# Optimization experiments

Measured on AMD Instinct MI355X. Metric: run time of the kernel, lower is better.

Reference implementation:

```python
import jax, jax.numpy as jnp
import numpy as np

# dims (see shape_source): seq S = d_t+1 must equal d_k for the unary quantum loader
B, T, D_IN = 128, 127, 48
DK = 128
S = T + 1            # tokens incl. class token; S == DK
H, L = 8, 6
P = (S * S - S) // 2  # RBS angles per head (pyramid circuit over S wires)


def _pyramid_pairs(n):
    # deterministic pyramid ordering of n(n-1)/2 adjacent-pair Givens rotations
    a, b = [], []
    for k in range(n - 1):
        for i in range(k, -1, -1):
            a.append(i)
            b.append(i + 1)
    return np.asarray(a, np.int32), np.asarray(b, np.int32)


def _build_W(phi, pa, pb, n):
    # classical simulation of the RBS pyramid circuit restricted to the unary
    # subspace: product of Givens rotations -> orthogonal n x n matrix
    def step(W, inp):
        ia, ib, th = inp
        c, s = jnp.cos(th), jnp.sin(th)
        ra, rb = W[ia], W[ib]
        W = W.at[ia].set(c * ra - s * rb)
        W = W.at[ib].set(s * ra + c * rb)
        return W, None
    W0 = jnp.eye(n, dtype=phi.dtype)
    W, _ = jax.lax.scan(step, W0, (pa, pb, phi))
    return W


def _layer_norm(x, g, b, eps=1e-5):
    m = jnp.mean(x, axis=-1, keepdims=True)
    v = jnp.mean((x - m) ** 2, axis=-1, keepdims=True)
    return (x - m) * jax.lax.rsqrt(v + eps) * g + b


def setup_inputs() -> dict:
    key = jax.random.key(0)
    ks = jax.random.split(key, 8)
    f32 = jnp.float32
    return {
        "x": jax.random.normal(ks[0], (B, T, D_IN), f32),
        "embed_w": jax.random.normal(ks[1], (DK, D_IN), f32) / np.sqrt(D_IN),
        "embed_b": jnp.zeros((DK,), f32),
        "class_token": jax.random.normal(ks[2], (DK,), f32) / DK,
        "norm0_g": jnp.ones((DK,), f32),
        "norm0_b": jnp.zeros((DK,), f32),
        "Vw": jax.random.normal(ks[3], (L, H, DK, DK), f32) / np.sqrt(DK),
        "Vb": jnp.zeros((L, H, DK), f32),
        "ln_g": jnp.ones((L, H, DK), f32),
        "ln_b": jnp.zeros((L, H, DK), f32),
        "phi": jax.random.normal(ks[4], (L, H, P), f32) / np.sqrt(S),
        "merger_w": jax.random.normal(ks[5], (L, H), f32) / np.sqrt(H),
        "merger_b": jnp.zeros((L,), f32),
    }


def reference(x, embed_w, embed_b, class_token, norm0_g, norm0_b,
              Vw, Vb, ln_g, ln_b, phi, merger_w, merger_b):
    Bsz = x.shape[0]
    pa, pb = _pyramid_pairs(S)
    # orthogonal score matrices for every (layer, head)
    Ws = jax.vmap(lambda p: _build_W(p, pa, pb, S))(phi.reshape(L * H, P))
    Ws = Ws.reshape(L, H, S, S)

    # embed patches, prepend class token (pos_embedding add is a no-op in the
    # original source: bare `+self.pos_embedding` statement, so it is omitted)
    tok = jnp.einsum('btf,df->btd', x, embed_w) + embed_b
    h = jnp.concatenate([jnp.broadcast_to(class_token, (Bsz, 1, DK)), tok], axis=1)
    h = _layer_norm(h, norm0_g, norm0_b)

    scale = 1.0 / np.sqrt(DK)
    for l in range(L):
        nrm = jnp.sqrt(jnp.sum(h * h, axis=-1))      # input3: token norms [B,S]
        u = h / nrm[..., None]                        # unit tokens (convert_array)
        hh, nn, uu = h, nrm, u

        def head(W, vw, vb, g, be):
            V = jnp.einsum('bsd,ed->bse', hh, vw) + vb
            M = jnp.einsum('bsd,de,bte->bst', uu, W, uu)
            A = (M * M) * (nn[:, :, None] * nn[:, None, :])
            Pm = jax.nn.softmax(A * scale, axis=-1)
            return _layer_norm(jnp.einsum('bst,btd->bsd', Pm, V) + hh, g, be)

        hs = jax.vmap(head)(Ws[l], Vw[l], Vb[l], ln_g[l], ln_b[l])  # [H,B,S,D]
        h = jnp.einsum('hbsd,h->bsd', hs, merger_w[l]) + merger_b[l]
    return h[:, -1, :]
```

## Files before the change

### kernel.cpp

```cpp
#include <hip/hip_runtime.h>
#include <hip/hip_bf16.h>


typedef __bf16 bf16x8 __attribute__((ext_vector_type(8)));
typedef float  f32x4  __attribute__((ext_vector_type(4)));
typedef unsigned int u32;

#define LDH 136

__global__ void __launch_bounds__(256)
vw_bf16_kernel(const float* __restrict__ vw, __bf16* __restrict__ cvw)
{
    int i = (blockIdx.x * 256 + threadIdx.x) * 4;
#pragma unroll
    for (int j = 0; j < 4; j++) cvw[i + j] = (__bf16)vw[i + j];
}

__global__ void __launch_bounds__(64)
sincos_kernel(const float* __restrict__ phi, float2* __restrict__ csn)
{
    const int mat = blockIdx.x / 254;
    const int t   = blockIdx.x % 254;
    const int j   = threadIdx.x;

    float th = 0.f;
    if (t < 253) {
        const int p = t & 1, i = 2 * j + p;
        const int lim = min(t, 252 - t);
        if (i <= lim) {
            const int k = (t + i) >> 1;
            th = phi[mat * 8128 + ((k * (k + 1)) >> 1) + (k - i)];
        }
    }
    float sn, cs;
    __sincosf(th, &sn, &cs);
    csn[(mat * 254 + t) * 64 + j] = make_float2(cs, sn);
}

__global__ void __launch_bounds__(64)
build_w_kernel(const float2* __restrict__ csn, __bf16* __restrict__ wt)
{
    const int mat = blockIdx.x >> 4;
    const int grp = blockIdx.x & 15;
    const int c0  = grp * 8;
    const int lam = threadIdx.x;

    const float2* base = csn + (mat * 254) * 64 + lam;

    float vlo[8], vhi[8];
#pragma unroll
    for (int j = 0; j < 8; j++) {
        vlo[j] = (2 * lam     == c0 + j) ? 1.f : 0.f;
        vhi[j] = (2 * lam + 1 == c0 + j) ? 1.f : 0.f;
    }

    float2 a  = base[0];
    float2 bq = base[64];

    for (int t = 0; t < 252; t += 2) {
        float2 c2 = base[(t + 2) * 64];
        float2 d2 = base[(t + 3) * 64];

        {
            const float cs = a.x, sn = a.y;
#pragma unroll
            for (int j = 0; j < 8; j++) {
                float lo = vlo[j], hi = vhi[j];
                vlo[j] = cs * lo - sn * hi;
                vhi[j] = sn * lo + cs * hi;
            }
        }
        {
            const float cs = bq.x, sn = bq.y;
#pragma unroll
            for (int j = 0; j < 8; j++) {
                float y  = __shfl_down(vlo[j], 1);
                float x  = vhi[j];
                float xn = cs * x - sn * y;
                float yn = sn * x + cs * y;
                vhi[j] = xn;
                float z = __shfl_up(yn, 1);
                if (lam > 0) vlo[j] = z;
            }
        }
        a = c2; bq = d2;
    }
    {
        const float cs = a.x, sn = a.y;
#pragma unroll
        for (int j = 0; j < 8; j++) {
            float lo = vlo[j], hi = vhi[j];
            vlo[j] = cs * lo - sn * hi;
            vhi[j] = sn * lo + cs * hi;
        }
    }

    u32* wtu = (u32*)wt;
#pragma unroll
    for (int j = 0; j < 8; j++) {
        __bf16 va = (__bf16)vlo[j];
        __bf16 vb = (__bf16)vhi[j];
        u32 pk = (u32)__builtin_bit_cast(unsigned short, va)
               | ((u32)__builtin_bit_cast(unsigned short, vb) << 16);
        wtu[mat * 8192 + (c0 + j) * 64 + lam] = pk;
    }
}

static __device__ __forceinline__ float block_sum_128(float v, float* sred)
{
#pragma unroll
    for (int m = 32; m; m >>= 1) v += __shfl_xor(v, m);
    __syncthreads();
    if ((threadIdx.x & 63) == 0) sred[threadIdx.x >> 6] = v;
    __syncthreads();
    return sred[0] + sred[1];
}

__global__ void __launch_bounds__(128)
embed_kernel(const float* __restrict__ x,  const float* __restrict__ ew,
             const float* __restrict__ eb, const float* __restrict__ ct,
             const float* __restrict__ g0, const float* __restrict__ b0,
             float* __restrict__ hf, __bf16* __restrict__ hb, float* __restrict__ invn)
{
    __shared__ float sx[48];
    __shared__ float sred[2];
    const int b = blockIdx.x & 127, s = blockIdx.x >> 7, d = threadIdx.x;

    float val;
    if (s == 0) {
        val = ct[d];
    } else {
        if (d < 48) sx[d] = x[(b * 127 + (s - 1)) * 48 + d];
        __syncthreads();
        float aa = 0.f;
#pragma unroll
        for (int f = 0; f < 48; f++) aa = fmaf(sx[f], ew[d * 48 + f], aa);
        val = aa + eb[d];
    }
    float mean = block_sum_128(val, sred) * (1.f / 128.f);
    float xc   = val - mean;
    float var  = block_sum_128(xc * xc, sred) * (1.f / 128.f);
    float y    = xc * rsqrtf(var + 1e-5f) * g0[d] + b0[d];
    float ss   = block_sum_128(y * y, sred);

    const int o = (b * 128 + s) * 128 + d;
    hf[o] = y;
    hb[o] = (__bf16)y;
    if (d == 0) invn[b * 128 + s] = rsqrtf(ss);
}

__global__ void __launch_bounds__(512, 2)
attn_kernel(int l,
            const float*  __restrict__ hf,  const __bf16* __restrict__ hb,
            const float*  __restrict__ invn, const __bf16* __restrict__ wt,
            const __bf16* __restrict__ vw,  const float* __restrict__ vb,
            const float* __restrict__ lng,  const float* __restrict__ lnb,
            const float* __restrict__ mwp,  __bf16* __restrict__ hs)
{
    __shared__ __align__(16) __bf16 sH[128 * LDH];
    __shared__ __align__(16) __bf16 sB[128 * LDH];
    __shared__ __align__(16) __bf16 sT[128 * LDH];
    __shared__ float sInv[128];
    __shared__ float sVb[128];
    __shared__ float sLg[128];
    __shared__ float sLb[128];

    const int tid  = threadIdx.x;
    const int lane = tid & 63, wave = tid >> 6;
    const int l15  = lane & 15, quad = lane >> 4;
    const int b    = blockIdx.x & 127;
    const int hh   = blockIdx.x >> 7;
    const int lh   = l * 8 + hh;

    const __bf16* hbp = hb + b * 16384;
    const __bf16* wtp = wt + lh * 16384;
    const __bf16* vwp = vw + lh * 16384;

    bf16x8 vwr[4];
#pragma unroll
    for (int c = 0; c < 4; c++) {
        int ch  = tid + c * 512;
        int row = ch >> 4, cc = ch & 15;
        bf16x8 hv = *(const bf16x8*)(hbp + ch * 8);
        bf16x8 wv = *(const bf16x8*)(wtp + ch * 8);
        vwr[c]    = *(const bf16x8*)(vwp + ch * 8);
        *(bf16x8*)(&sH[row * LDH + cc * 8]) = hv;
        *(bf16x8*)(&sB[row * LDH + cc * 8]) = wv;
    }
    if (tid < 128) {
        sInv[tid] = invn[b * 128 + tid];
        sVb[tid]  = vb[lh * 128 + tid];
        sLg[tid]  = lng[lh * 128 + tid];
        sLb[tid]  = lnb[lh * 128 + tid];
    }
    __syncthreads();

    const int rowA = wave * 16 + l15;
    const int kq   = quad * 8;
    const int srow = wave * 16 + quad * 4;
    const f32x4 vzero = {0.f, 0.f, 0.f, 0.f};

    f32x4 acc[8];

#pragma unroll
    for (int t = 0; t < 8; t++) acc[t] = vzero;
#pragma unroll
    for (int k0 = 0; k0 < 128; k0 += 32) {
        bf16x8 af = *(const bf16x8*)(&sH[rowA * LDH + k0 + kq]);
#pragma unroll
        for (int t = 0; t < 8; t++) {
            bf16x8 bfr = *(const bf16x8*)(&sB[(t * 16 + l15) * LDH + k0 + kq]);
            acc[t] = __builtin_amdgcn_mfma_f32_16x16x32_bf16(af, bfr, acc[t], 0, 0, 0);
        }
    }
#pragma unroll
    for (int t = 0; t < 8; t++)
#pragma unroll
        for (int r = 0; r < 4; r++)
            sT[(srow + r) * LDH + t * 16 + l15] = (__bf16)acc[t][r];

    __syncthreads();

#pragma unroll
    for (int c = 0; c < 4; c++) {
        int ch = tid + c * 512; int row = ch >> 4, cc = ch & 15;
        *(bf16x8*)(&sB[row * LDH + cc * 8]) = vwr[c];
    }

#pragma unroll
    for (int t = 0; t < 8; t++) acc[t] = vzero;
#pragma unroll
    for (int k0 = 0; k0 < 128; k0 += 32) {
        bf16x8 af = *(const bf16x8*)(&sT[rowA * LDH + k0 + kq]);
#pragma unroll
        for (int t = 0; t < 8; t++) {
            bf16x8 bfr = *(const bf16x8*)(&sH[(t * 16 + l15) * LDH + k0 + kq]);
            acc[t] = __builtin_amdgcn_mfma_f32_16x16x32_bf16(af, bfr, acc[t], 0, 0, 0);
        }
    }

    {
        const float scale = 0.08838834764831843f;
        float invs[4], invt[8];
#pragma unroll
        for (int r = 0; r < 4; r++) invs[r] = sInv[srow + r];
#pragma unroll
        for (int t = 0; t < 8; t++) invt[t] = sInv[t * 16 + l15];

        float mx[4] = {-3e38f, -3e38f, -3e38f, -3e38f};
#pragma unroll
        for (int t = 0; t < 8; t++)
#pragma unroll
            for (int r = 0; r < 4; r++) {
                float g = acc[t][r];
                float v = g * g * invs[r] * invt[t] * scale;
                acc[t][r] = v;
                mx[r] = fmaxf(mx[r], v);
            }
#pragma unroll
        for (int m = 1; m < 16; m <<= 1)
#pragma unroll
            for (int r = 0; r < 4; r++) mx[r] = fmaxf(mx[r], __shfl_xor(mx[r], m));

        float sm[4] = {0.f, 0.f, 0.f, 0.f};
#pragma unroll
        for (int t = 0; t < 8; t++)
#pragma unroll
            for (int r = 0; r < 4; r++) {
                float e = __expf(acc[t][r] - mx[r]);
                acc[t][r] = e;
                sm[r] += e;
            }
#pragma unroll
        for (int m = 1; m < 16; m <<= 1)
#pragma unroll
            for (int r = 0; r < 4; r++) sm[r] += __shfl_xor(sm[r], m);
#pragma unroll
        for (int r = 0; r < 4; r++) sm[r] = 1.0f / sm[r];
#pragma unroll
        for (int t = 0; t < 8; t++)
#pragma unroll
            for (int r = 0; r < 4; r++)
                sT[(srow + r) * LDH + t * 16 + l15] = (__bf16)(acc[t][r] * sm[r]);
    }

    float hres[8][4];
    {
        const float* hfp = hf + (b * 128 + srow) * 128;
#pragma unroll
        for (int t = 0; t < 8; t++)
#pragma unroll
            for (int r = 0; r < 4; r++)
                hres[t][r] = hfp[r * 128 + t * 16 + l15];
    }

    __syncthreads();

#pragma unroll
    for (int t = 0; t < 8; t++) acc[t] = vzero;
#pragma unroll
    for (int k0 = 0; k0 < 128; k0 += 32) {
        bf16x8 af = *(const bf16x8*)(&sH[rowA * LDH + k0 + kq]);
#pragma unroll
        for (int t = 0; t < 8; t++) {
            bf16x8 bfr = *(const bf16x8*)(&sB[(t * 16 + l15) * LDH + k0 + kq]);
            acc[t] = __builtin_amdgcn_mfma_f32_16x16x32_bf16(af, bfr, acc[t], 0, 0, 0);
        }
    }
    __syncthreads();

    {
        float vbv[8];
#pragma unroll
        for (int t = 0; t < 8; t++) vbv[t] = sVb[t * 16 + l15];
#pragma unroll
        for (int t = 0; t < 8; t++)
#pragma unroll
            for (int r = 0; r < 4; r++)
                sH[(t * 16 + l15) * LDH + srow + r] = (__bf16)(acc[t][r] + vbv[t]);
    }
    __syncthreads();

#pragma unroll
    for (int t = 0; t < 8; t++) acc[t] = vzero;
#pragma unroll
    for (int k0 = 0; k0 < 128; k0 += 32) {
        bf16x8 af = *(const bf16x8*)(&sT[rowA * LDH + k0 + kq]);
#pragma unroll
        for (int t = 0; t < 8; t++) {
            bf16x8 bfr = *(const bf16x8*)(&sH[(t * 16 + l15) * LDH + k0 + kq]);
            acc[t] = __builtin_amdgcn_mfma_f32_16x16x32_bf16(af, bfr, acc[t], 0, 0, 0);
        }
    }

    {
        const float mw = mwp[lh];
        float sum_[4] = {0.f, 0.f, 0.f, 0.f};
        float sq_[4]  = {0.f, 0.f, 0.f, 0.f};
#pragma unroll
        for (int t = 0; t < 8; t++)
#pragma unroll
            for (int r = 0; r < 4; r++) {
                float x = acc[t][r] + hres[t][r];
                acc[t][r] = x;
                sum_[r] += x;
                sq_[r]  += x * x;
            }
#pragma unroll
        for (int m = 1; m < 16; m <<= 1)
#pragma unroll
            for (int r = 0; r < 4; r++) {
                sum_[r] += __shfl_xor(sum_[r], m);
                sq_[r]  += __shfl_xor(sq_[r], m);
            }
        float mean[4], rstd[4];
#pragma unroll
        for (int r = 0; r < 4; r++) {
            mean[r] = sum_[r] * (1.f / 128.f);
            float var = sq_[r] * (1.f / 128.f) - mean[r] * mean[r];
            rstd[r] = rsqrtf(fmaxf(var, 0.f) + 1e-5f);
        }
        float lgv[8], lbv[8];
#pragma unroll
        for (int t = 0; t < 8; t++) {
            lgv[t] = sLg[t * 16 + l15];
            lbv[t] = sLb[t * 16 + l15];
        }
        __bf16* hsp = hs + ((hh * 128 + b) * 128 + srow) * 128;
#pragma unroll
        for (int t = 0; t < 8; t++)
#pragma unroll
            for (int r = 0; r < 4; r++) {
                float y = (acc[t][r] - mean[r]) * rstd[r] * lgv[t] + lbv[t];
                hsp[r * 128 + t * 16 + l15] = (__bf16)(y * mw);
            }
    }
}

__global__ void __launch_bounds__(128)
merge_kernel(const __bf16* __restrict__ hs, const float* __restrict__ mbp, int l,
             float* __restrict__ hf, __bf16* __restrict__ hb, float* __restrict__ invn,
             float* __restrict__ out, int last)
{
    __shared__ float sred[2];
    const int b = blockIdx.x & 127, s = blockIdx.x >> 7, d = threadIdx.x;

    float acc = mbp[l];
#pragma unroll
    for (int h = 0; h < 8; h++)
        acc += (float)hs[((h * 128 + b) * 128 + s) * 128 + d];

    float ss = block_sum_128(acc * acc, sred);

    const int o = (b * 128 + s) * 128 + d;
    hf[o] = acc;
    hb[o] = (__bf16)acc;
    if (d == 0) invn[b * 128 + s] = rsqrtf(ss);
    if (last && s == 127) out[b * 128 + d] = acc;
}

extern "C" void kernel_launch(void* const* d_in, const int* in_sizes, int n_in,
                              void* d_out, int out_size, void* d_ws, size_t ws_size,
                              hipStream_t stream)
{
    (void)in_sizes; (void)n_in; (void)out_size; (void)ws_size;

    const float* x   = (const float*)d_in[0];
    const float* ew  = (const float*)d_in[1];
    const float* eb  = (const float*)d_in[2];
    const float* ct  = (const float*)d_in[3];
    const float* g0  = (const float*)d_in[4];
    const float* b0  = (const float*)d_in[5];
    const float* vw  = (const float*)d_in[6];
    const float* vb  = (const float*)d_in[7];
    const float* lng = (const float*)d_in[8];
    const float* lnb = (const float*)d_in[9];
    const float* phi = (const float*)d_in[10];
    const float* mw  = (const float*)d_in[11];
    const float* mb  = (const float*)d_in[12];
    float* out = (float*)d_out;

    char* ws = (char*)d_ws;
    __bf16* wt   = (__bf16*)(ws);
    float*  hf   = (float*)(ws + 1572864);
    __bf16* hb   = (__bf16*)(ws + 9961472);
    float*  invn = (float*)(ws + 14155776);
    __bf16* hs   = (__bf16*)(ws + 14221312);
    __bf16* cvw  = (__bf16*)(ws + 47775744);
    float2* csn  = (float2*)(ws + 49348608);

    vw_bf16_kernel<<<768, 256, 0, stream>>>(vw, cvw);
    sincos_kernel<<<48 * 254, 64, 0, stream>>>(phi, csn);
    build_w_kernel<<<768, 64, 0, stream>>>(csn, wt);
    embed_kernel<<<16384, 128, 0, stream>>>(x, ew, eb, ct, g0, b0, hf, hb, invn);
    for (int l = 0; l < 6; l++) {
        attn_kernel<<<1024, 512, 0, stream>>>(l, hf, hb, invn, wt, cvw, vb,
                                              lng, lnb, mw, hs);
        merge_kernel<<<16384, 128, 0, stream>>>(hs, mb, l, hf, hb, invn, out,
                                                (l == 5) ? 1 : 0);
    }
}
```

Baseline: 470.5 us.

## Use 4-wave blocks with 32-row tiles, XOR-swizzled LDS, and head-major block order

The attention kernel now runs with 256 threads, and each wave computes two 16-row MFMA tiles that share every B-fragment load, halving B reads from LDS per MFMA. The padded LDS layout is replaced by an XOR swizzle to avoid bank conflicts without padding. Block indexing is changed so the 8 heads of one batch run in adjacent blocks, which should improve L2 reuse of hb/hf. In exchange there are fewer waves per block and more accumulator registers per thread (hres and acc both double), which may reduce occupancy.

After: 533.4 us. 13.4% more time.

```diff
diff --git a/kernel.cpp b/kernel.cpp
--- a/kernel.cpp
+++ b/kernel.cpp
@@ -6,7 +6,10 @@
 typedef float  f32x4  __attribute__((ext_vector_type(4)));
 typedef unsigned int u32;
 
-#define LDH 136
+__device__ __forceinline__ int sidx(int row, int col)
+{
+    return row * 128 + ((((col >> 3) ^ (row & 15)) << 3) | (col & 7));
+}
 
 __global__ void __launch_bounds__(256)
 vw_bf16_kernel(const float* __restrict__ vw, __bf16* __restrict__ cvw)
@@ -60,7 +63,6 @@
     for (int t = 0; t < 252; t += 2) {
         float2 c2 = base[(t + 2) * 64];
         float2 d2 = base[(t + 3) * 64];
-
         {
             const float cs = a.x, sn = a.y;
 #pragma unroll
@@ -149,7 +151,7 @@
     if (d == 0) invn[b * 128 + s] = rsqrtf(ss);
 }
 
-__global__ void __launch_bounds__(512, 2)
+__global__ void __launch_bounds__(256, 1)
 attn_kernel(int l,
             const float*  __restrict__ hf,  const __bf16* __restrict__ hb,
             const float*  __restrict__ invn, const __bf16* __restrict__ wt,
@@ -157,35 +159,35 @@
             const float* __restrict__ lng,  const float* __restrict__ lnb,
             const float* __restrict__ mwp,  __bf16* __restrict__ hs)
 {
-    __shared__ __align__(16) __bf16 sH[128 * LDH];
-    __shared__ __align__(16) __bf16 sB[128 * LDH];
-    __shared__ __align__(16) __bf16 sT[128 * LDH];
+    __shared__ __align__(16) __bf16 sH[128 * 128];
+    __shared__ __align__(16) __bf16 sB[128 * 128];
+    __shared__ __align__(16) __bf16 sT[128 * 128];
     __shared__ float sInv[128];
     __shared__ float sVb[128];
     __shared__ float sLg[128];
     __shared__ float sLb[128];
 
     const int tid  = threadIdx.x;
-    const int lane = tid & 63, wave = tid >> 6;
+    const int lane = tid & 63, w = tid >> 6;
     const int l15  = lane & 15, quad = lane >> 4;
-    const int b    = blockIdx.x & 127;
-    const int hh   = blockIdx.x >> 7;
+    const int hh   = blockIdx.x & 7;
+    const int b    = blockIdx.x >> 3;
     const int lh   = l * 8 + hh;
 
     const __bf16* hbp = hb + b * 16384;
     const __bf16* wtp = wt + lh * 16384;
     const __bf16* vwp = vw + lh * 16384;
 
-    bf16x8 vwr[4];
-#pragma unroll
-    for (int c = 0; c < 4; c++) {
-        int ch  = tid + c * 512;
+    bf16x8 vwr[8];
+#pragma unroll
+    for (int c = 0; c < 8; c++) {
+        int ch  = tid + c * 256;
         int row = ch >> 4, cc = ch & 15;
         bf16x8 hv = *(const bf16x8*)(hbp + ch * 8);
         bf16x8 wv = *(const bf16x8*)(wtp + ch * 8);
         vwr[c]    = *(const bf16x8*)(vwp + ch * 8);
-        *(bf16x8*)(&sH[row * LDH + cc * 8]) = hv;
-        *(bf16x8*)(&sB[row * LDH + cc * 8]) = wv;
+        *(bf16x8*)(&sH[sidx(row, cc * 8)]) = hv;
+        *(bf16x8*)(&sB[sidx(row, cc * 8)]) = wv;
     }
     if (tid < 128) {
         sInv[tid] = invn[b * 128 + tid];
@@ -195,118 +197,116 @@
     }
     __syncthreads();
 
-    const int rowA = wave * 16 + l15;
+    const int r0   = w * 32;
     const int kq   = quad * 8;
-    const int srow = wave * 16 + quad * 4;
+    const int q4   = quad * 4;
     const f32x4 vzero = {0.f, 0.f, 0.f, 0.f};
 
-    f32x4 acc[8];
-
-#pragma unroll
-    for (int t = 0; t < 8; t++) acc[t] = vzero;
-#pragma unroll
-    for (int k0 = 0; k0 < 128; k0 += 32) {
-        bf16x8 af = *(const bf16x8*)(&sH[rowA * LDH + k0 + kq]);
-#pragma unroll
-        for (int t = 0; t < 8; t++) {
-            bf16x8 bfr = *(const bf16x8*)(&sB[(t * 16 + l15) * LDH + k0 + kq]);
-            acc[t] = __builtin_amdgcn_mfma_f32_16x16x32_bf16(af, bfr, acc[t], 0, 0, 0);
-        }
-    }
-#pragma unroll
-    for (int t = 0; t < 8; t++)
-#pragma unroll
-        for (int r = 0; r < 4; r++)
-            sT[(srow + r) * LDH + t * 16 + l15] = (__bf16)acc[t][r];
-
-    __syncthreads();
-
-#pragma unroll
-    for (int c = 0; c < 4; c++) {
-        int ch = tid + c * 512; int row = ch >> 4, cc = ch & 15;
-        *(bf16x8*)(&sB[row * LDH + cc * 8]) = vwr[c];
-    }
-
-#pragma unroll
-    for (int t = 0; t < 8; t++) acc[t] = vzero;
-#pragma unroll
-    for (int k0 = 0; k0 < 128; k0 += 32) {
-        bf16x8 af = *(const bf16x8*)(&sT[rowA * LDH + k0 + kq]);
-#pragma unroll
-        for (int t = 0; t < 8; t++) {
-            bf16x8 bfr = *(const bf16x8*)(&sH[(t * 16 + l15) * LDH + k0 + kq]);
-            acc[t] = __builtin_amdgcn_mfma_f32_16x16x32_bf16(af, bfr, acc[t], 0, 0, 0);
-        }
-    }
+    f32x4 acc[2][8];
+
+    auto mm = [&](const __bf16* Ab, const __bf16* Bb) {
+#pragma unroll
+        for (int rt = 0; rt < 2; rt++)
+#pragma unroll
+            for (int t = 0; t < 8; t++) acc[rt][t] = vzero;
+#pragma unroll
+        for (int k0 = 0; k0 < 128; k0 += 32) {
+            const int kk = k0 + kq;
+            bf16x8 a0 = *(const bf16x8*)(&Ab[sidx(r0 + l15, kk)]);
+            bf16x8 a1 = *(const bf16x8*)(&Ab[sidx(r0 + 16 + l15, kk)]);
+#pragma unroll
+            for (int t = 0; t < 8; t++) {
+                bf16x8 bb = *(const bf16x8*)(&Bb[sidx(t * 16 + l15, kk)]);
+                acc[0][t] = __builtin_amdgcn_mfma_f32_16x16x32_bf16(a0, bb, acc[0][t], 0, 0, 0);
+                acc[1][t] = __builtin_amdgcn_mfma_f32_16x16x32_bf16(a1, bb, acc[1][t], 0, 0, 0);
+            }
+        }
+    };
+
+    mm(sH, sB);
+#pragma unroll
+    for (int rt = 0; rt < 2; rt++)
+#pragma unroll
+        for (int t = 0; t < 8; t++)
+#pragma unroll
+            for (int r = 0; r < 4; r++)
+                sT[sidx(r0 + rt * 16 + q4 + r, t * 16 + l15)] = (__bf16)acc[rt][t][r];
+
+    __syncthreads();
+
+#pragma unroll
+    for (int c = 0; c < 8; c++) {
+        int ch = tid + c * 256; int row = ch >> 4, cc = ch & 15;
+        *(bf16x8*)(&sB[sidx(row, cc * 8)]) = vwr[c];
+    }
+
+    mm(sT, sH);
 
     {
         const float scale = 0.08838834764831843f;
-        float invs[4], invt[8];
-#pragma unroll
-        for (int r = 0; r < 4; r++) invs[r] = sInv[srow + r];
+        float invt[8];
 #pragma unroll
         for (int t = 0; t < 8; t++) invt[t] = sInv[t * 16 + l15];
 
-        float mx[4] = {-3e38f, -3e38f, -3e38f, -3e38f};
+#pragma unroll
+        for (int rt = 0; rt < 2; rt++) {
+            float invs[4];
+#pragma unroll
+            for (int r = 0; r < 4; r++) invs[r] = sInv[r0 + rt * 16 + q4 + r];
+
+            float mx[4] = {-3e38f, -3e38f, -3e38f, -3e38f};
+#pragma unroll
+            for (int t = 0; t < 8; t++)
+#pragma unroll
+                for (int r = 0; r < 4; r++) {
+                    float g = acc[rt][t][r];
+                    float v = g * g * invs[r] * invt[t] * scale;
+                    acc[rt][t][r] = v;
+                    mx[r] = fmaxf(mx[r], v);
+                }
+#pragma unroll
+            for (int m = 1; m < 16; m <<= 1)
+#pragma unroll
+                for (int r = 0; r < 4; r++) mx[r] = fmaxf(mx[r], __shfl_xor(mx[r], m));
+
+            float sm[4] = {0.f, 0.f, 0.f, 0.f};
+#pragma unroll
+            for (int t = 0; t < 8; t++)
+#pragma unroll
+                for (int r = 0; r < 4; r++) {
+                    float e = __expf(acc[rt][t][r] - mx[r]);
+                    acc[rt][t][r] = e;
+                    sm[r] += e;
+                }
+#pragma unroll
+            for (int m = 1; m < 16; m <<= 1)
+#pragma unroll
+                for (int r = 0; r < 4; r++) sm[r] += __shfl_xor(sm[r], m);
+#pragma unroll
+            for (int r = 0; r < 4; r++) sm[r] = 1.0f / sm[r];
+#pragma unroll
+            for (int t = 0; t < 8; t++)
+#pragma unroll
+                for (int r = 0; r < 4; r++)
+                    sT[sidx(r0 + rt * 16 + q4 + r, t * 16 + l15)] =
+                        (__bf16)(acc[rt][t][r] * sm[r]);
+        }
+    }
+
+    float hres[2][8][4];
+#pragma unroll
+    for (int rt = 0; rt < 2; rt++) {
+        const float* hfp = hf + (b * 128 + r0 + rt * 16 + q4) * 128;
 #pragma unroll
         for (int t = 0; t < 8; t++)
 #pragma unroll
-            for (int r = 0; r < 4; r++) {
-                float g = acc[t][r];
-                float v = g * g * invs[r] * invt[t] * scale;
-                acc[t][r] = v;
-                mx[r] = fmaxf(mx[r], v);
-            }
-#pragma unroll
-        for (int m = 1; m < 16; m <<= 1)
-#pragma unroll
-            for (int r = 0; r < 4; r++) mx[r] = fmaxf(mx[r], __shfl_xor(mx[r], m));
-
-        float sm[4] = {0.f, 0.f, 0.f, 0.f};
-#pragma unroll
-        for (int t = 0; t < 8; t++)
-#pragma unroll
-            for (int r = 0; r < 4; r++) {
-                float e = __expf(acc[t][r] - mx[r]);
-                acc[t][r] = e;
-                sm[r] += e;
-            }
-#pragma unroll
-        for (int m = 1; m < 16; m <<= 1)
-#pragma unroll
-            for (int r = 0; r < 4; r++) sm[r] += __shfl_xor(sm[r], m);
-#pragma unroll
-        for (int r = 0; r < 4; r++) sm[r] = 1.0f / sm[r];
-#pragma unroll
-        for (int t = 0; t < 8; t++)
-#pragma unroll
             for (int r = 0; r < 4; r++)
-                sT[(srow + r) * LDH + t * 16 + l15] = (__bf16)(acc[t][r] * sm[r]);
-    }
-
-    float hres[8][4];
-    {
-        const float* hfp = hf + (b * 128 + srow) * 128;
-#pragma unroll
-        for (int t = 0; t < 8; t++)
-#pragma unroll
-            for (int r = 0; r < 4; r++)
-                hres[t][r] = hfp[r * 128 + t * 16 + l15];
-    }
-
-    __syncthreads();
-
-#pragma unroll
-    for (int t = 0; t < 8; t++) acc[t] = vzero;
-#pragma unroll
-    for (int k0 = 0; k0 < 128; k0 += 32) {
-        bf16x8 af = *(const bf16x8*)(&sH[rowA * LDH + k0 + kq]);
-#pragma unroll
-        for (int t = 0; t < 8; t++) {
-            bf16x8 bfr = *(const bf16x8*)(&sB[(t * 16 + l15) * LDH + k0 + kq]);
-            acc[t] = __builtin_amdgcn_mfma_f32_16x16x32_bf16(af, bfr, acc[t], 0, 0, 0);
-        }
-    }
+                hres[rt][t][r] = hfp[r * 128 + t * 16 + l15];
+    }
+
+    __syncthreads();
+
+    mm(sH, sB);
     __syncthreads();
 
     {
@@ -314,66 +314,62 @@
 #pragma unroll
         for (int t = 0; t < 8; t++) vbv[t] = sVb[t * 16 + l15];
 #pragma unroll
-        for (int t = 0; t < 8; t++)
-#pragma unroll
-            for (int r = 0; r < 4; r++)
-                sH[(t * 16 + l15) * LDH + srow + r] = (__bf16)(acc[t][r] + vbv[t]);
-    }
-    __syncthreads();
-
-#pragma unroll
-    for (int t = 0; t < 8; t++) acc[t] = vzero;
-#pragma unroll
-    for (int k0 = 0; k0 < 128; k0 += 32) {
-        bf16x8 af = *(const bf16x8*)(&sT[rowA * LDH + k0 + kq]);
-#pragma unroll
-        for (int t = 0; t < 8; t++) {
-            bf16x8 bfr = *(const bf16x8*)(&sH[(t * 16 + l15) * LDH + k0 + kq]);
-            acc[t] = __builtin_amdgcn_mfma_f32_16x16x32_bf16(af, bfr, acc[t], 0, 0, 0);
-        }
-    }
+        for (int rt = 0; rt < 2; rt++)
+#pragma unroll
+            for (int t = 0; t < 8; t++)
+#pragma unroll
+                for (int r = 0; r < 4; r++)
+                    sH[sidx(t * 16 + l15, r0 + rt * 16 + q4 + r)] =
+                        (__bf16)(acc[rt][t][r] + vbv[t]);
+    }
+    __syncthreads();
+
+    mm(sT, sH);
 
     {
         const float mw = mwp[lh];
-        float sum_[4] = {0.f, 0.f, 0.f, 0.f};
-        float sq_[4]  = {0.f, 0.f, 0.f, 0.f};
-#pragma unroll
-        for (int t = 0; t < 8; t++)
-#pragma unroll
-            for (int r = 0; r < 4; r++) {
-                float x = acc[t][r] + hres[t][r];
-                acc[t][r] = x;
-                sum_[r] += x;
-                sq_[r]  += x * x;
-            }
-#pragma unroll
-        for (int m = 1; m < 16; m <<= 1)
-#pragma unroll
-            for (int r = 0; r < 4; r++) {
-                sum_[r] += __shfl_xor(sum_[r], m);
-                sq_[r]  += __shfl_xor(sq_[r], m);
-            }
-        float mean[4], rstd[4];
-#pragma unroll
-        for (int r = 0; r < 4; r++) {
-            mean[r] = sum_[r] * (1.f / 128.f);
-            float var = sq_[r] * (1.f / 128.f) - mean[r] * mean[r];
-            rstd[r] = rsqrtf(fmaxf(var, 0.f) + 1e-5f);
-        }
         float lgv[8], lbv[8];
 #pragma unroll
         for (int t = 0; t < 8; t++) {
             lgv[t] = sLg[t * 16 + l15];
             lbv[t] = sLb[t * 16 + l15];
         }
-        __bf16* hsp = hs + ((hh * 128 + b) * 128 + srow) * 128;
-#pragma unroll
-        for (int t = 0; t < 8; t++)
+#pragma unroll
+        for (int rt = 0; rt < 2; rt++) {
+            float sum_[4] = {0.f, 0.f, 0.f, 0.f};
+            float sq_[4]  = {0.f, 0.f, 0.f, 0.f};
+#pragma unroll
+            for (int t = 0; t < 8; t++)
+#pragma unroll
+                for (int r = 0; r < 4; r++) {
+                    float xx = acc[rt][t][r] + hres[rt][t][r];
+                    acc[rt][t][r] = xx;
+                    sum_[r] += xx;
+                    sq_[r]  += xx * xx;
+                }
+#pragma unroll
+            for (int m = 1; m < 16; m <<= 1)
+#pragma unroll
+                for (int r = 0; r < 4; r++) {
+                    sum_[r] += __shfl_xor(sum_[r], m);
+                    sq_[r]  += __shfl_xor(sq_[r], m);
+                }
+            float mean[4], rstd[4];
 #pragma unroll
             for (int r = 0; r < 4; r++) {
-                float y = (acc[t][r] - mean[r]) * rstd[r] * lgv[t] + lbv[t];
-                hsp[r * 128 + t * 16 + l15] = (__bf16)(y * mw);
+                mean[r] = sum_[r] * (1.f / 128.f);
+                float var = sq_[r] * (1.f / 128.f) - mean[r] * mean[r];
+                rstd[r] = rsqrtf(fmaxf(var, 0.f) + 1e-5f);
             }
+            __bf16* hsp = hs + ((hh * 128 + b) * 128 + r0 + rt * 16 + q4) * 128;
+#pragma unroll
+            for (int t = 0; t < 8; t++)
+#pragma unroll
+                for (int r = 0; r < 4; r++) {
+                    float y = (acc[rt][t][r] - mean[r]) * rstd[r] * lgv[t] + lbv[t];
+                    hsp[r * 128 + t * 16 + l15] = (__bf16)(y * mw);
+                }
+        }
     }
 }
 
@@ -434,7 +430,7 @@
     build_w_kernel<<<768, 64, 0, stream>>>(csn, wt);
     embed_kernel<<<16384, 128, 0, stream>>>(x, ew, eb, ct, g0, b0, hf, hb, invn);
     for (int l = 0; l < 6; l++) {
-        attn_kernel<<<1024, 512, 0, stream>>>(l, hf, hb, invn, wt, cvw, vb,
+        attn_kernel<<<1024, 256, 0, stream>>>(l, hf, hb, invn, wt, cvw, vb,
                                               lng, lnb, mw, hs);
         merge_kernel<<<16384, 128, 0, stream>>>(hs, mb, l, hf, hb, invn, out,
                                                 (l == 5) ? 1 : 0);
```
